# Kernel optimization log

Measured on AMD Instinct MI355X. Metric: run time of the kernel, lower is better.

## Reference

```python
import jax, jax.numpy as jnp
import numpy as np

K = 8
LOCAL_WINDOW_RATIO = 0.25
NEG = -1e9
LN_EPS = 1e-5
NORM_EPS = 1e-12


def _window_indices(H, W):
    lws = max(3, int(min(H, W) * LOCAL_WINDOW_RATIO))
    if lws % 2 == 0:
        lws += 1
    half = lws // 2
    off = jnp.arange(-half, half + 1)
    dy, dx = jnp.meshgrid(off, off, indexing='ij')          # [lws,lws]
    dy = dy.reshape(-1); dx = dx.reshape(-1)                 # [w2]
    py, px = jnp.meshgrid(jnp.arange(H), jnp.arange(W), indexing='ij')
    py = py.reshape(-1); px = px.reshape(-1)                 # [HW]
    ny = py[:, None] + dy[None, :]                           # [HW,w2]
    nx = px[:, None] + dx[None, :]
    valid = (ny >= 0) & (ny < H) & (nx >= 0) & (nx < W)
    idx = jnp.clip(ny, 0, H - 1) * W + jnp.clip(nx, 0, W - 1)
    return idx, valid


def setup_inputs() -> dict:
    key = jax.random.key(0)
    ks = jax.random.split(key, 5)
    B, C, H, W = 4, 96, 48, 48
    return {
        'x': jax.random.normal(ks[0], (B, C, H, W), jnp.float32),
        'w1': jax.random.normal(ks[1], (2 * C, C), jnp.float32) * 0.05,
        'b1': jax.random.normal(ks[2], (2 * C,), jnp.float32) * 0.05,
        'w2': jax.random.normal(ks[3], (C, 2 * C), jnp.float32) * 0.05,
        'b2': jax.random.normal(ks[4], (C,), jnp.float32) * 0.05,
        'ln_w': jnp.ones((C,), jnp.float32),
        'ln_b': jnp.zeros((C,), jnp.float32),
    }


def reference(x, w1, b1, w2, b2, ln_w, ln_b):
    B, C, H, W = x.shape
    HW = H * W
    idx_w, valid = _window_indices(H, W)                     # [HW,w2]

    x_flat = x.transpose(0, 2, 3, 1).reshape(B, HW, C)       # [B,HW,C]
    n = jnp.linalg.norm(x_flat, axis=-1, keepdims=True)
    x_n = x_flat / jnp.maximum(n, NORM_EPS)

    win_n = x_n[:, idx_w, :]                                 # [B,HW,w2,C]
    sims = jnp.einsum('bpc,bpwc->bpw', x_n, win_n)           # cosine sim
    sims = jnp.where(valid[None], sims, NEG)

    # every pixel has >= (half+1)^2 >= K valid neighbors, so top-k stays valid
    top_sim, top_idx = jax.lax.top_k(sims, K)                # [B,HW,K]
    wts = jax.nn.softmax(top_sim, axis=-1)                   # exp/sum over top-k

    idx_g = jnp.take_along_axis(jnp.broadcast_to(idx_w[None], sims.shape), top_idx, axis=-1)  # [B,HW,K]
    feats = x_flat[jnp.arange(B)[:, None, None], idx_g]      # [B,HW,K,C] (un-normalized)
    agg = jnp.einsum('bpk,bpkc->bpc', wts, feats)            # [B,HW,C]

    mu = jnp.mean(x_flat, axis=-1, keepdims=True)
    var = jnp.var(x_flat, axis=-1, keepdims=True)
    x_ln = (x_flat - mu) / jnp.sqrt(var + LN_EPS) * ln_w + ln_b

    enhanced = agg + x_ln                                    # [B,HW,C]
    h = jax.nn.relu(jnp.einsum('bpc,dc->bpd', enhanced, w1) + b1)
    ffn = jnp.einsum('bpd,cd->bpc', h, w2) + b2
    out = enhanced + ffn
    return out.reshape(B, H, W, C).transpose(0, 3, 1, 2)
```

## Files before the change

### kernel.cpp

```cpp
#include <hip/hip_runtime.h>
#include <math.h>

#define BATCH 4
#define CH    96
#define HH    48
#define WW    48
#define HWPIX (HH*WW)
#define NPIX  (BATCH*HWPIX)
#define WIN   13
#define WIN2  169
#define HALF  6
#define TOPK  8
#define NEGV  (-1000000000.0f)

__global__ __launch_bounds__(256) void k0_wt(
    const float* __restrict__ w1, const float* __restrict__ w2,
    float* __restrict__ w1T, float* __restrict__ w2T)
{
    __shared__ float tile[32][33];
    int bid = blockIdx.x;
    const float* src; float* dst; int R, C, tr, tc;
    if (bid < 18) { src = w1; dst = w1T; R = 192; C = 96;  tr = bid / 3; tc = bid % 3; }
    else { int b2 = bid - 18; src = w2; dst = w2T; R = 96; C = 192; tr = b2 / 6; tc = b2 % 6; }
    int r0 = tr * 32, c0 = tc * 32;
    int tx = threadIdx.x & 31, ty = threadIdx.x >> 5;

    #pragma unroll
    for (int i = 0; i < 4; ++i) {
        int r = ty + i * 8;
        tile[r][tx] = src[(r0 + r) * C + c0 + tx];
    }
    __syncthreads();
    #pragma unroll
    for (int i = 0; i < 4; ++i) {
        int r = ty + i * 8;
        dst[(c0 + r) * R + r0 + tx] = tile[tx][r];
    }
}

__global__ __launch_bounds__(256) void k1_prep(
    const float* __restrict__ x, float* __restrict__ xt2,
    float* __restrict__ invn, float* __restrict__ muv, float* __restrict__ rsd)
{
    __shared__ float lds[96][17];
    int bid = blockIdx.x;
    int b   = bid / 144;
    int p0  = (bid % 144) * 16;
    int t   = threadIdx.x;

    #pragma unroll
    for (int it = 0; it < 6; ++it) {
        int e = t + it * 256;
        int c = e >> 4;
        int p = e & 15;
        lds[c][p] = x[(b * CH + c) * HWPIX + p0 + p];
    }
    __syncthreads();

    if (t < 16) {
        float s = 0.f, ss = 0.f;
        #pragma unroll
        for (int c = 0; c < CH; ++c) { float v = lds[c][t]; s += v; ss += v * v; }
        int gpix = b * HWPIX + p0 + t;
        invn[gpix] = 1.0f / fmaxf(sqrtf(ss), 1e-12f);
        float m = s * (1.0f / 96.0f);
        muv[gpix] = m;
        rsd[gpix] = rsqrtf(ss * (1.0f / 96.0f) - m * m + 1e-5f);
    }

    float4* x4 = (float4*)xt2;
    for (int i = t; i < 384; i += 256) {
        int p = i & 15;
        int s = i >> 4;
        float4 v = make_float4(lds[4*s][p], lds[4*s+1][p],
                               lds[4*s+2][p], lds[4*s+3][p]);
        x4[s * NPIX + b * HWPIX + p0 + p] = v;
    }
}

__global__ __launch_bounds__(256, 4) void k2_knn(
    const float* __restrict__ xt2, const float* __restrict__ invn,
    const float* __restrict__ muv, const float* __restrict__ rsd,
    const float* __restrict__ lnw, const float* __restrict__ lnb,
    float* __restrict__ enh)
{
    __shared__ float own[4][96];
    int t    = threadIdx.x;
    int wv   = t >> 6;
    int lane = t & 63;
    int gp   = blockIdx.x * 4 + wv;
    int b    = gp / HWPIX;
    int p    = gp - b * HWPIX;
    int py   = p / WW;
    int px   = p - py * WW;
    const float4* x4 = (const float4*)xt2;

    float4 ownv = make_float4(0.f, 0.f, 0.f, 0.f);
    if (lane < 24) {
        ownv = x4[lane * NPIX + gp];
        ((float4*)(own[wv]))[lane] = ownv;
    }
    float inp = invn[gp];
    float mu  = muv[gp];
    float rs  = rsd[gp];

    float v0 = -2e9f, v1 = -2e9f, v2 = -2e9f;
    const float4* ov = (const float4*)(own[wv]);
    #pragma unroll
    for (int k = 0; k < 3; ++k) {
        int n = lane + 64 * k;
        float sim = -2e9f;
        if (n < WIN2) {
            int dy = n / WIN - HALF;
            int dx = n - (dy + HALF) * WIN - HALF;
            int ny = py + dy, nx = px + dx;
            if (ny >= 0 && ny < HH && nx >= 0 && nx < WW) {
                int q = b * HWPIX + ny * WW + nx;
                float inq = invn[q];
                const float4* rp = x4 + q;
                float ax = 0.f, ay = 0.f, az = 0.f, aw = 0.f;
                #pragma unroll
                for (int s = 0; s < 24; ++s) {
                    float4 a  = ov[s];
                    float4 bb = rp[s * NPIX];
                    ax += a.x * bb.x; ay += a.y * bb.y;
                    az += a.z * bb.z; aw += a.w * bb.w;
                }
                sim = ((ax + ay) + (az + aw)) * inp * inq;
            } else {
                sim = NEGV;
            }
        }
        if (k == 0) v0 = sim; else if (k == 1) v1 = sim; else v2 = sim;
    }

    float tv[TOPK]; int tn[TOPK];
    #pragma unroll
    for (int r = 0; r < TOPK; ++r) {
        float m = fmaxf(fmaxf(v0, v1), v2);
        #pragma unroll
        for (int off = 1; off < 64; off <<= 1)
            m = fmaxf(m, __shfl_xor(m, off));
        unsigned long long m0 = __ballot(v0 == m);
        unsigned long long m1 = __ballot(v1 == m);
        unsigned long long m2 = __ballot(v2 == m);
        int n;
        if (m0)      n = (int)__builtin_ctzll(m0);
        else if (m1) n = 64 + (int)__builtin_ctzll(m1);
        else         n = 128 + (int)__builtin_ctzll(m2);
        tv[r] = m; tn[r] = n;
        int kk = n >> 6, ll = n & 63;
        if (ll == lane) {
            if (kk == 0)      v0 = -2e9f;
            else if (kk == 1) v1 = -2e9f;
            else              v2 = -2e9f;
        }
    }

    float wts[TOPK]; int qn[TOPK];
    float wsum = 0.f;
    #pragma unroll
    for (int r = 0; r < TOPK; ++r) {
        float e = expf(tv[r] - tv[0]);
        wts[r] = e; wsum += e;
        int n  = tn[r];
        int dy = n / WIN - HALF;
        int dx = n - (dy + HALF) * WIN - HALF;
        int gy = min(max(py + dy, 0), HH - 1);
        int gx = min(max(px + dx, 0), WW - 1);
        qn[r]  = b * HWPIX + gy * WW + gx;
    }
    float winv = 1.0f / wsum;

    if (lane < 24) {
        const float4* base = x4 + lane * NPIX;
        float4 g = make_float4(0.f, 0.f, 0.f, 0.f);
        #pragma unroll
        for (int r = 0; r < TOPK; ++r) {
            float4 f = base[qn[r]];
            float w = wts[r];
            g.x += w * f.x; g.y += w * f.y;
            g.z += w * f.z; g.w += w * f.w;
        }
        float4 lw = ((const float4*)lnw)[lane];
        float4 lb = ((const float4*)lnb)[lane];
        float4 e;
        e.x = g.x * winv + (ownv.x - mu) * rs * lw.x + lb.x;
        e.y = g.y * winv + (ownv.y - mu) * rs * lw.y + lb.y;
        e.z = g.z * winv + (ownv.z - mu) * rs * lw.z + lb.z;
        e.w = g.w * winv + (ownv.w - mu) * rs * lw.w + lb.w;
        ((float4*)(enh + gp * CH))[lane] = e;
    }
}

__global__ __launch_bounds__(192, 4) void k3_ffn(
    const float* __restrict__ enh, const float* __restrict__ w1T,
    const float* __restrict__ b1, const float* __restrict__ w2T,
    const float* __restrict__ b2, float* __restrict__ out)
{
    __shared__ float hl[8][200];
    int g  = blockIdx.x;
    int b  = g / 288;
    int p0 = (g % 288) * 8;
    int t  = threadIdx.x;
    const float4* ebase = (const float4*)(enh + (b * HWPIX + p0) * CH);

    {
        int j = t;
        float a0=0.f,a1=0.f,a2=0.f,a3=0.f,a4=0.f,a5=0.f,a6=0.f,a7=0.f;
        #pragma unroll 4
        for (int c4 = 0; c4 < 24; ++c4) {
            float wa = w1T[(4*c4 + 0) * 192 + j];
            float wb = w1T[(4*c4 + 1) * 192 + j];
            float wc = w1T[(4*c4 + 2) * 192 + j];
            float wd = w1T[(4*c4 + 3) * 192 + j];
            float4 v0 = ebase[0*24 + c4];
            float4 v1 = ebase[1*24 + c4];
            float4 v2 = ebase[2*24 + c4];
            float4 v3 = ebase[3*24 + c4];
            float4 v4 = ebase[4*24 + c4];
            float4 v5 = ebase[5*24 + c4];
            float4 v6 = ebase[6*24 + c4];
            float4 v7 = ebase[7*24 + c4];
            a0 += v0.x*wa + v0.y*wb + v0.z*wc + v0.w*wd;
            a1 += v1.x*wa + v1.y*wb + v1.z*wc + v1.w*wd;
            a2 += v2.x*wa + v2.y*wb + v2.z*wc + v2.w*wd;
            a3 += v3.x*wa + v3.y*wb + v3.z*wc + v3.w*wd;
            a4 += v4.x*wa + v4.y*wb + v4.z*wc + v4.w*wd;
            a5 += v5.x*wa + v5.y*wb + v5.z*wc + v5.w*wd;
            a6 += v6.x*wa + v6.y*wb + v6.z*wc + v6.w*wd;
            a7 += v7.x*wa + v7.y*wb + v7.z*wc + v7.w*wd;
        }
        float bj = b1[j];
        hl[0][j] = fmaxf(a0 + bj, 0.f);
        hl[1][j] = fmaxf(a1 + bj, 0.f);
        hl[2][j] = fmaxf(a2 + bj, 0.f);
        hl[3][j] = fmaxf(a3 + bj, 0.f);
        hl[4][j] = fmaxf(a4 + bj, 0.f);
        hl[5][j] = fmaxf(a5 + bj, 0.f);
        hl[6][j] = fmaxf(a6 + bj, 0.f);
        hl[7][j] = fmaxf(a7 + bj, 0.f);
    }
    __syncthreads();

    {
        int c    = (t >= 96) ? t - 96 : t;
        int half = (t >= 96) ? 1 : 0;
        int q0p  = half * 4;
        const float4* h0 = (const float4*)(&hl[q0p    ][0]);
        const float4* h1 = (const float4*)(&hl[q0p + 1][0]);
        const float4* h2 = (const float4*)(&hl[q0p + 2][0]);
        const float4* h3 = (const float4*)(&hl[q0p + 3][0]);
        float s0 = 0.f, s1 = 0.f, s2 = 0.f, s3 = 0.f;
        #pragma unroll 6
        for (int j4 = 0; j4 < 48; ++j4) {
            float wa = w2T[(4*j4 + 0) * 96 + c];
            float wb = w2T[(4*j4 + 1) * 96 + c];
            float wc = w2T[(4*j4 + 2) * 96 + c];
            float wd = w2T[(4*j4 + 3) * 96 + c];
            float4 u0 = h0[j4], u1 = h1[j4], u2 = h2[j4], u3 = h3[j4];
            s0 += u0.x*wa + u0.y*wb + u0.z*wc + u0.w*wd;
            s1 += u1.x*wa + u1.y*wb + u1.z*wc + u1.w*wd;
            s2 += u2.x*wa + u2.y*wb + u2.z*wc + u2.w*wd;
            s3 += u3.x*wa + u3.y*wb + u3.z*wc + u3.w*wd;
        }
        float bc = b2[c];
        int pb = p0 + q0p;
        out[(b * CH + c) * HWPIX + pb + 0] =
            enh[(b * HWPIX + pb + 0) * CH + c] + s0 + bc;
        out[(b * CH + c) * HWPIX + pb + 1] =
            enh[(b * HWPIX + pb + 1) * CH + c] + s1 + bc;
        out[(b * CH + c) * HWPIX + pb + 2] =
            enh[(b * HWPIX + pb + 2) * CH + c] + s2 + bc;
        out[(b * CH + c) * HWPIX + pb + 3] =
            enh[(b * HWPIX + pb + 3) * CH + c] + s3 + bc;
    }
}

extern "C" void kernel_launch(void* const* d_in, const int* in_sizes, int n_in,
                              void* d_out, int out_size, void* d_ws, size_t ws_size,
                              hipStream_t stream)
{
    const float* x   = (const float*)d_in[0];
    const float* w1  = (const float*)d_in[1];
    const float* b1  = (const float*)d_in[2];
    const float* w2  = (const float*)d_in[3];
    const float* b2  = (const float*)d_in[4];
    const float* lnw = (const float*)d_in[5];
    const float* lnb = (const float*)d_in[6];
    float* out = (float*)d_out;

    float* xt2 = out;

    float* ws   = (float*)d_ws;
    float* enh  = ws;
    float* invn = enh + NPIX * CH;
    float* muv  = invn + NPIX;
    float* rsd  = muv + NPIX;
    float* w1T  = rsd + NPIX;
    float* w2T  = w1T + 192 * 96;

    hipLaunchKernelGGL(k0_wt, dim3(36), dim3(256), 0, stream,
                       w1, w2, w1T, w2T);
    hipLaunchKernelGGL(k1_prep, dim3(576), dim3(256), 0, stream,
                       x, xt2, invn, muv, rsd);
    hipLaunchKernelGGL(k2_knn, dim3(NPIX / 4), dim3(256), 0, stream,
                       xt2, invn, muv, rsd, lnw, lnb, enh);
    hipLaunchKernelGGL(k3_ffn, dim3(1152), dim3(192), 0, stream,
                       enh, w1T, b1, w2T, b2, out);
}
```

Before: 79.45 us.

## Stage shared 14x14 neighbor window in LDS for 2x2 pixel tiles in kNN kernel

The kNN kernel now assigns each block a 2x2 pixel tile and cooperatively loads the union 14x14 neighborhood (in two 48-channel halves) into shared memory, so the four pixels' 169-neighbor dot products read from LDS instead of issuing strided global loads per neighbor. Out-of-image cells are zero-filled and masked by precomputed validity flags. The change is meant to cut redundant global and L2 traffic from overlapping windows. In exchange it uses about 37 KB of LDS per block and adds syncs, and the launch-bounds occupancy hints are dropped from both the kNN and FFN kernels.

```diff
diff --git a/kernel.cpp b/kernel.cpp
--- a/kernel.cpp
+++ b/kernel.cpp
@@ -13,6 +13,9 @@
 #define TOPK  8
 #define NEGV  (-1000000000.0f)
 
+#define WROW  14
+#define WCELL 196
+
 __global__ __launch_bounds__(256) void k0_wt(
     const float* __restrict__ w1, const float* __restrict__ w2,
     float* __restrict__ w1T, float* __restrict__ w2T)
@@ -78,61 +81,86 @@
     }
 }
 
-__global__ __launch_bounds__(256, 4) void k2_knn(
+__global__ __launch_bounds__(256) void k2_knn(
     const float* __restrict__ xt2, const float* __restrict__ invn,
     const float* __restrict__ muv, const float* __restrict__ rsd,
     const float* __restrict__ lnw, const float* __restrict__ lnb,
     float* __restrict__ enh)
 {
-    __shared__ float own[4][96];
+    __shared__ float4 wtile[12 * WCELL];
     int t    = threadIdx.x;
     int wv   = t >> 6;
     int lane = t & 63;
-    int gp   = blockIdx.x * 4 + wv;
-    int b    = gp / HWPIX;
-    int p    = gp - b * HWPIX;
-    int py   = p / WW;
-    int px   = p - py * WW;
+    int blk  = blockIdx.x;
+    int b    = blk / 576;
+    int tid  = blk % 576;
+    int ty0  = (tid / 24) * 2;
+    int tx0  = (tid % 24) * 2;
+    int ly   = wv >> 1, lx = wv & 1;
+    int py   = ty0 + ly, px = tx0 + lx;
+    int gp   = b * HWPIX + py * WW + px;
     const float4* x4 = (const float4*)xt2;
 
-    float4 ownv = make_float4(0.f, 0.f, 0.f, 0.f);
-    if (lane < 24) {
-        ownv = x4[lane * NPIX + gp];
-        ((float4*)(own[wv]))[lane] = ownv;
+    int r0, r1, r2;  bool ok0, ok1, ok2;  int q0, q1, q2;
+    {
+        int n, dy, dx, ny, nx;
+        n = lane;        dy = n / WIN; dx = n - dy * WIN;
+        r0 = (ly + dy) * WROW + (lx + dx);
+        ny = py + dy - HALF; nx = px + dx - HALF;
+        ok0 = (ny >= 0) && (ny < HH) && (nx >= 0) && (nx < WW);
+        q0  = b * HWPIX + min(max(ny,0),HH-1) * WW + min(max(nx,0),WW-1);
+        n = lane + 64;   dy = n / WIN; dx = n - dy * WIN;
+        r1 = (ly + dy) * WROW + (lx + dx);
+        ny = py + dy - HALF; nx = px + dx - HALF;
+        ok1 = (ny >= 0) && (ny < HH) && (nx >= 0) && (nx < WW);
+        q1  = b * HWPIX + min(max(ny,0),HH-1) * WW + min(max(nx,0),WW-1);
+        n = lane + 128;  dy = n / WIN; dx = n - dy * WIN;
+        bool in2 = (n < WIN2);
+        int rr = (ly + dy) * WROW + (lx + dx);
+        r2 = in2 ? rr : r0;
+        ny = py + dy - HALF; nx = px + dx - HALF;
+        ok2 = in2 && (ny >= 0) && (ny < HH) && (nx >= 0) && (nx < WW);
+        q2  = in2 ? (b * HWPIX + min(max(ny,0),HH-1) * WW + min(max(nx,0),WW-1)) : q0;
     }
     float inp = invn[gp];
     float mu  = muv[gp];
     float rs  = rsd[gp];
-
-    float v0 = -2e9f, v1 = -2e9f, v2 = -2e9f;
-    const float4* ov = (const float4*)(own[wv]);
-    #pragma unroll
-    for (int k = 0; k < 3; ++k) {
-        int n = lane + 64 * k;
-        float sim = -2e9f;
-        if (n < WIN2) {
-            int dy = n / WIN - HALF;
-            int dx = n - (dy + HALF) * WIN - HALF;
-            int ny = py + dy, nx = px + dx;
-            if (ny >= 0 && ny < HH && nx >= 0 && nx < WW) {
-                int q = b * HWPIX + ny * WW + nx;
-                float inq = invn[q];
-                const float4* rp = x4 + q;
-                float ax = 0.f, ay = 0.f, az = 0.f, aw = 0.f;
-                #pragma unroll
-                for (int s = 0; s < 24; ++s) {
-                    float4 a  = ov[s];
-                    float4 bb = rp[s * NPIX];
-                    ax += a.x * bb.x; ay += a.y * bb.y;
-                    az += a.z * bb.z; aw += a.w * bb.w;
-                }
-                sim = ((ax + ay) + (az + aw)) * inp * inq;
-            } else {
-                sim = NEGV;
-            }
-        }
-        if (k == 0) v0 = sim; else if (k == 1) v1 = sim; else v2 = sim;
-    }
+    float in0 = invn[q0], in1 = invn[q1], in2v = invn[q2];
+    int r_own = (ly + HALF) * WROW + (lx + HALF);
+
+    float a0x=0.f,a0y=0.f,a0z=0.f,a0w=0.f;
+    float a1x=0.f,a1y=0.f,a1z=0.f,a1w=0.f;
+    float a2x=0.f,a2y=0.f,a2z=0.f,a2w=0.f;
+
+    #pragma unroll
+    for (int h = 0; h < 2; ++h) {
+        if (h) __syncthreads();
+        for (int i = t; i < 12 * WCELL; i += 256) {
+            int r  = i % WCELL;
+            int sc = i / WCELL;
+            int gy = ty0 - HALF + r / WROW;
+            int gx = tx0 - HALF + r % WROW;
+            float4 v = make_float4(0.f, 0.f, 0.f, 0.f);
+            if (gy >= 0 && gy < HH && gx >= 0 && gx < WW)
+                v = x4[(h * 12 + sc) * NPIX + b * HWPIX + gy * WW + gx];
+            wtile[sc * WCELL + r] = v;
+        }
+        __syncthreads();
+
+        #pragma unroll 4
+        for (int s = 0; s < 12; ++s) {
+            float4 o  = wtile[s * WCELL + r_own];
+            float4 b0 = wtile[s * WCELL + r0];
+            float4 b1 = wtile[s * WCELL + r1];
+            float4 b2 = wtile[s * WCELL + r2];
+            a0x += o.x*b0.x; a0y += o.y*b0.y; a0z += o.z*b0.z; a0w += o.w*b0.w;
+            a1x += o.x*b1.x; a1y += o.y*b1.y; a1z += o.z*b1.z; a1w += o.w*b1.w;
+            a2x += o.x*b2.x; a2y += o.y*b2.y; a2z += o.z*b2.z; a2w += o.w*b2.w;
+        }
+    }
+    float v0 = ok0 ? ((a0x+a0y)+(a0z+a0w)) * inp * in0  : NEGV;
+    float v1 = ok1 ? ((a1x+a1y)+(a1z+a1w)) * inp * in1  : NEGV;
+    float v2 = ok2 ? ((a2x+a2y)+(a2z+a2w)) * inp * in2v : NEGV;
 
     float tv[TOPK]; int tn[TOPK];
     #pragma unroll
@@ -173,6 +201,7 @@
     float winv = 1.0f / wsum;
 
     if (lane < 24) {
+        float4 ownv = x4[lane * NPIX + gp];
         const float4* base = x4 + lane * NPIX;
         float4 g = make_float4(0.f, 0.f, 0.f, 0.f);
         #pragma unroll
@@ -193,7 +222,7 @@
     }
 }
 
-__global__ __launch_bounds__(192, 4) void k3_ffn(
+__global__ __launch_bounds__(192) void k3_ffn(
     const float* __restrict__ enh, const float* __restrict__ w1T,
     const float* __restrict__ b1, const float* __restrict__ w2T,
     const float* __restrict__ b2, float* __restrict__ out)
@@ -304,7 +333,7 @@
                        w1, w2, w1T, w2T);
     hipLaunchKernelGGL(k1_prep, dim3(576), dim3(256), 0, stream,
                        x, xt2, invn, muv, rsd);
-    hipLaunchKernelGGL(k2_knn, dim3(NPIX / 4), dim3(256), 0, stream,
+    hipLaunchKernelGGL(k2_knn, dim3(2304), dim3(256), 0, stream,
                        xt2, invn, muv, rsd, lnw, lnb, enh);
     hipLaunchKernelGGL(k3_ffn, dim3(1152), dim3(192), 0, stream,
                        enh, w1T, b1, w2T, b2, out);
```

Measured after the change: 83.38 us. +5.0%, slower.
